# Kernel tuning notes

Measured on AMD Instinct MI355X. Metric: run time of the kernel, lower is better.

The kernel has to match this reference:

```python
import jax, jax.numpy as jnp
import numpy as np
import math

B, W, BINS, H, K = 1, 2048, 1024, 16, 3  # batch, seq (==cropsize), bins, num_bands, kernel


def setup_inputs() -> dict:
    key = jax.random.key(0)
    ks = jax.random.split(key, 7)
    s = 1.0 / math.sqrt(BINS)
    x = jax.random.normal(ks[0], (B, W, BINS), jnp.float32)
    wq = jax.random.normal(ks[1], (BINS, BINS), jnp.float32) * s
    wk = jax.random.normal(ks[2], (BINS, BINS), jnp.float32) * s
    wv = jax.random.normal(ks[3], (BINS, BINS), jnp.float32) * s
    wo = jax.random.normal(ks[4], (BINS, BINS), jnp.float32) * s
    conv_w = jax.random.normal(ks[5], (BINS, 1, K), jnp.float32) * (1.0 / math.sqrt(K))  # depthwise
    er = jax.random.normal(ks[6], (BINS // H, W), jnp.float32)  # relative-position embeddings
    return {"x": x, "wq": wq, "wk": wk, "wv": wv, "wo": wo, "conv_w": conv_w, "er": er}


def _dwconv(x_bwc, w):
    # depthwise Conv1d, 'same' padding (pad=1, k=3). x: [b,w,c], kernel: [c,1,K]
    y = jax.lax.conv_general_dilated(
        x_bwc.transpose(0, 2, 1), w, window_strides=(1,), padding=[(1, 1)],
        feature_group_count=x_bwc.shape[-1], dimension_numbers=("NCH", "OIH", "NCH"))
    return y.transpose(0, 2, 1)


def reference(x, wq, wk, wv, wo, conv_w, er):
    b, w, c = x.shape
    h = H
    d = c // h
    # NOTE: original torch code applies q_conv to q, k AND v (k_conv/v_conv unused).
    q = _dwconv(x @ wq, conv_w).reshape(b, w, h, d).transpose(0, 2, 1, 3)   # [b,h,w,d]
    k = _dwconv(x @ wk, conv_w).reshape(b, w, h, d).transpose(0, 2, 3, 1)   # [b,h,d,w]
    v = _dwconv(x @ wv, conv_w).reshape(b, w, h, d).transpose(0, 2, 1, 3)   # [b,h,w,d]
    # relative-position skewing trick (Music-Transformer style)
    qe = jnp.einsum("bhwd,dr->bhwr", q, er)                                  # [b,h,w,cropsize]
    p = jnp.pad(qe, ((0, 0), (0, 0), (0, 0), (1, 0))).transpose(0, 1, 3, 2)[:, :, 1:, :]  # [b,h,w,w]
    qk = (jnp.einsum("bhwd,bhdk->bhwk", q, k) + p) / math.sqrt(c)
    a = jax.nn.softmax(qk, axis=-1)
    out = jnp.einsum("bhwk,bhkd->bhwd", a, v).transpose(0, 2, 1, 3).reshape(b, w, c)
    return out @ wo
```

## Files before the change

### kernel.cpp

```cpp
#include <hip/hip_runtime.h>
#include <hip/hip_bf16.h>

typedef __attribute__((ext_vector_type(8))) short short8;
typedef __attribute__((ext_vector_type(4))) float floatx4;

__device__ __forceinline__ float bf2f(unsigned short b) {
    union { unsigned int u; float f; } v; v.u = ((unsigned int)b) << 16; return v.f;
}
__device__ __forceinline__ unsigned short f2bf(float f) {
    union { float f; unsigned int u; } v; v.f = f;
    unsigned int r = v.u + 0x7fffu + ((v.u >> 16) & 1u);
    return (unsigned short)(r >> 16);
}
__device__ __forceinline__ unsigned int pk2bf(float a, float b) {
    __hip_bfloat162 h = __float22bfloat162_rn(make_float2(a, b));
    union { __hip_bfloat162 h; unsigned int u; } v; v.h = h; return v.u;
}

union Pack16 { uint4 v[2]; unsigned short u[16]; };
__device__ __forceinline__ void cvt16(const float* __restrict__ src, float s, Pack16& t) {
    float tmp[16];
    *(float4*)&tmp[0]  = ((const float4*)src)[0];
    *(float4*)&tmp[4]  = ((const float4*)src)[1];
    *(float4*)&tmp[8]  = ((const float4*)src)[2];
    *(float4*)&tmp[12] = ((const float4*)src)[3];
#pragma unroll
    for (int i = 0; i < 16; i++) t.u[i] = f2bf(tmp[i] * s);
}

#define MFMA16(a, b, c) __builtin_amdgcn_mfma_f32_16x16x32_bf16((a), (b), (c), 0, 0, 0)

template<bool A_F32, bool BT_PRE, bool C_F32>
__global__ __launch_bounds__(256) void gemm128(
    const void* __restrict__ Ap,
    const void* __restrict__ B0, const void* __restrict__ B1, const void* __restrict__ B2,
    void* __restrict__ C0, void* __restrict__ C1, void* __restrict__ C2,
    int M, int N, int K)
{
    __shared__ __align__(16) unsigned short As[128][72];
    __shared__ __align__(16) unsigned short Bs[128][72];
    const int tid = threadIdx.x;
    const int sel = blockIdx.x >> 3;
    const int n0  = (blockIdx.x & 7) * 128;
    const int m0  = blockIdx.y * 128;
    const void* Bp = (sel == 0) ? B0 : (sel == 1) ? B1 : B2;
    void*       Cp = (sel == 0) ? C0 : (sel == 1) ? C1 : C2;

    const int wv = tid >> 6, lane = tid & 63;
    const int quad = lane >> 4, l15 = lane & 15;
    const int wm0 = (wv >> 1) * 64, wn0 = (wv & 1) * 64;

    floatx4 acc[4][4] = {};

    for (int k0 = 0; k0 < K; k0 += 64) {
        __syncthreads();
        {
            const int r = tid >> 2, c = (tid & 3) * 16;
#pragma unroll
            for (int p = 0; p < 2; p++) {
                const int row = p * 64 + r;
                if (A_F32) {
                    Pack16 t;
                    cvt16((const float*)Ap + (size_t)(m0 + row) * K + k0 + c, 1.0f, t);
                    *(uint4*)&As[row][c]     = t.v[0];
                    *(uint4*)&As[row][c + 8] = t.v[1];
                } else {
                    const uint4* a = (const uint4*)((const unsigned short*)Ap +
                                                    (size_t)(m0 + row) * K + k0 + c);
                    uint4 x0 = a[0], x1 = a[1];
                    *(uint4*)&As[row][c]     = x0;
                    *(uint4*)&As[row][c + 8] = x1;
                }
            }
        }
        if (BT_PRE) {
            const int r = tid >> 2, c = (tid & 3) * 16;
#pragma unroll
            for (int p = 0; p < 2; p++) {
                const int row = p * 64 + r;
                const uint4* b = (const uint4*)((const unsigned short*)Bp +
                                                (size_t)(n0 + row) * K + k0 + c);
                uint4 x0 = b[0], x1 = b[1];
                *(uint4*)&Bs[row][c]     = x0;
                *(uint4*)&Bs[row][c + 8] = x1;
            }
        } else {
            const int kr = tid >> 2, nb = (tid & 3) * 32;
            float t[32];
            const float* b = (const float*)Bp + (size_t)(k0 + kr) * N + n0 + nb;
#pragma unroll
            for (int i = 0; i < 8; i++) *(float4*)&t[i * 4] = ((const float4*)b)[i];
            const int col = ((kr >> 3) ^ ((nb >> 5) & 3)) * 8 + (kr & 7);
#pragma unroll
            for (int j = 0; j < 32; j++) Bs[nb + j][col] = f2bf(t[j]);
        }
        __syncthreads();

#pragma unroll
        for (int ks = 0; ks < 2; ks++) {
            const int kc = ks * 32 + quad * 8;
            short8 af[4], bfr[4];
#pragma unroll
            for (int i = 0; i < 4; i++)
                af[i] = *(const short8*)&As[wm0 + i * 16 + l15][kc];
#pragma unroll
            for (int i = 0; i < 4; i++) {
                int bcol;
                if (BT_PRE) bcol = kc;
                else {
                    const int cx = ((wn0 + i * 16) >> 5) & 3;
                    bcol = ((ks * 4 + quad) ^ cx) * 8;
                }
                bfr[i] = *(const short8*)&Bs[wn0 + i * 16 + l15][bcol];
            }
#pragma unroll
            for (int mt = 0; mt < 4; mt++)
#pragma unroll
                for (int nt = 0; nt < 4; nt++)
                    acc[mt][nt] = MFMA16(af[mt], bfr[nt], acc[mt][nt]);
        }
    }

#pragma unroll
    for (int mt = 0; mt < 4; mt++)
#pragma unroll
        for (int nt = 0; nt < 4; nt++)
#pragma unroll
            for (int r = 0; r < 4; r++) {
                const int row = m0 + wm0 + mt * 16 + quad * 4 + r;
                const int col = n0 + wn0 + nt * 16 + l15;
                if (C_F32)
                    ((float*)Cp)[(size_t)row * N + col] = acc[mt][nt][r];
                else
                    ((unsigned short*)Cp)[(size_t)row * N + col] = f2bf(acc[mt][nt][r]);
            }
}

__global__ __launch_bounds__(256) void wtrans(
    const float* __restrict__ W, unsigned short* __restrict__ WT, int Kd, int Nd)
{
    __shared__ __align__(16) unsigned short T[64][72];
    const int tid = threadIdx.x;
    const int n0 = blockIdx.x * 64, k0 = blockIdx.y * 64;
    {
        const int kr = tid >> 2, nc = (tid & 3) * 16;
        Pack16 t;
        cvt16(W + (size_t)(k0 + kr) * Nd + n0 + nc, 1.0f, t);
#pragma unroll
        for (int j = 0; j < 16; j++) T[nc + j][kr] = t.u[j];
    }
    __syncthreads();
    {
        const int nr = tid >> 2, kc = (tid & 3) * 16;
        uint4 x0 = *(const uint4*)&T[nr][kc];
        uint4 x1 = *(const uint4*)&T[nr][kc + 8];
        uint4* dst = (uint4*)(WT + (size_t)(n0 + nr) * Kd + k0 + kc);
        dst[0] = x0; dst[1] = x1;
    }
}

__global__ __launch_bounds__(256) void conv_qk(
    const unsigned short* __restrict__ in, const float* __restrict__ cw,
    unsigned short* __restrict__ out)
{
    const int idx = blockIdx.x * 256 + threadIdx.x;
    const int w = idx >> 7, c0 = (idx & 127) * 8;
    union { uint4 v; unsigned short u[8]; } a = {}, b, c = {};
    b.v = *(const uint4*)(in + (size_t)w * 1024 + c0);
    if (w > 0)    a.v = *(const uint4*)(in + (size_t)(w - 1) * 1024 + c0);
    if (w < 2047) c.v = *(const uint4*)(in + (size_t)(w + 1) * 1024 + c0);
    union { uint4 v; unsigned short u[8]; } o;
#pragma unroll
    for (int i = 0; i < 8; i++) {
        const float* k3 = cw + (size_t)(c0 + i) * 3;
        o.u[i] = f2bf(bf2f(a.u[i]) * k3[0] + bf2f(b.u[i]) * k3[1] + bf2f(c.u[i]) * k3[2]);
    }
    *(uint4*)(out + (size_t)w * 1024 + c0) = o.v;
}

__global__ __launch_bounds__(256) void conv_vt(
    const unsigned short* __restrict__ in, const float* __restrict__ cw,
    unsigned short* __restrict__ vT)
{
    __shared__ __align__(16) unsigned short T[64][72];
    const int tid = threadIdx.x;
    const int w0 = blockIdx.x * 64, h = blockIdx.y;
    {
        const int wr = tid >> 2, c4 = (tid & 3) * 16;
        const int cg = h * 64 + c4;
        const int w = w0 + wr;
        union { uint4 v[2]; unsigned short u[16]; } a = {}, b, c = {};
        b.v[0] = *(const uint4*)(in + (size_t)w * 1024 + cg);
        b.v[1] = *(const uint4*)(in + (size_t)w * 1024 + cg + 8);
        if (w > 0) {
            a.v[0] = *(const uint4*)(in + (size_t)(w - 1) * 1024 + cg);
            a.v[1] = *(const uint4*)(in + (size_t)(w - 1) * 1024 + cg + 8);
        }
        if (w < 2047) {
            c.v[0] = *(const uint4*)(in + (size_t)(w + 1) * 1024 + cg);
            c.v[1] = *(const uint4*)(in + (size_t)(w + 1) * 1024 + cg + 8);
        }
#pragma unroll
        for (int i = 0; i < 16; i++) {
            const float* k3 = cw + (size_t)(cg + i) * 3;
            T[c4 + i][wr] = f2bf(bf2f(a.u[i]) * k3[0] + bf2f(b.u[i]) * k3[1] +
                                 bf2f(c.u[i]) * k3[2]);
        }
    }
    __syncthreads();
    {
        const int dr = tid >> 2, w4 = (tid & 3) * 16;
        uint4 x0 = *(const uint4*)&T[dr][w4];
        uint4 x1 = *(const uint4*)&T[dr][w4 + 8];
        uint4* dst = (uint4*)(vT + (size_t)(h * 64 + dr) * 2048 + w0 + w4);
        dst[0] = x0; dst[1] = x1;
    }
}

__global__ __launch_bounds__(256, 2) void attn16(
    const unsigned short* __restrict__ qc, const unsigned short* __restrict__ kc,
    const unsigned short* __restrict__ vT, const float* __restrict__ er,
    unsigned short* __restrict__ outp)
{
    __shared__ __align__(16) unsigned char smem[70720];
    unsigned short* Qp = (unsigned short*)smem;

    const int tid = threadIdx.x;
    const int q0 = blockIdx.x * 64, h = blockIdx.y;
    const int wv = tid >> 6, lane = tid & 63;
    const int quad = lane >> 4, l15 = lane & 15;
    const float sc2 = 0.03125f * 1.44269504f;

    {
        const int m = tid >> 2, c4 = (tid & 3) * 16;
        union { uint4 v[2]; unsigned short u[16]; } t;
        t.v[0] = *(const uint4*)(qc + (size_t)(q0 + m) * 1024 + h * 64 + c4);
        t.v[1] = *(const uint4*)(qc + (size_t)(q0 + m) * 1024 + h * 64 + c4 + 8);
#pragma unroll
        for (int i = 0; i < 16; i++) t.u[i] = f2bf(bf2f(t.u[i]) * sc2);
        *(uint4*)&Qp[m * 136 + c4]     = t.v[0];
        *(uint4*)&Qp[m * 136 + c4 + 8] = t.v[1];
        Pack16 e;
        cvt16(er + (size_t)m * 2048 + q0 + c4, sc2, e);
#pragma unroll
        for (int j = 0; j < 16; j++) Qp[(c4 + j) * 136 + 64 + m] = e.u[j];
    }
    __syncthreads();

    short8 Bq[4][4];
#pragma unroll
    for (int qm = 0; qm < 4; qm++)
#pragma unroll
        for (int ks = 0; ks < 4; ks++)
            Bq[qm][ks] = *(const short8*)&Qp[(qm * 16 + l15) * 136 + ks * 32 + quad * 8];

    unsigned short* Ps = (unsigned short*)(smem + 17408 + wv * 9216);

    floatx4 oacc[4][4] = {};
    float lp[4] = {0.f, 0.f, 0.f, 0.f};

    for (int i = 0; i < 8; i++) {
        const int kt = 4 * i + wv;
        floatx4 s[4][4] = {};
#pragma unroll
        for (int half = 0; half < 2; half++) {
            short8 Af[2][4];
#pragma unroll
            for (int kmh = 0; kmh < 2; kmh++)
#pragma unroll
                for (int ks = 0; ks < 4; ks++) {
                    const int row = kt * 64 + (half * 2 + kmh) * 16 + l15;
                    const unsigned short* src = (ks < 2) ? kc : qc;
                    const int col = h * 64 + (ks & 1) * 32 + quad * 8;
                    Af[kmh][ks] = *(const short8*)(src + (size_t)row * 1024 + col);
                }
#pragma unroll
            for (int ks = 0; ks < 4; ks++)
#pragma unroll
                for (int kmh = 0; kmh < 2; kmh++)
#pragma unroll
                    for (int qm = 0; qm < 4; qm++)
                        s[half * 2 + kmh][qm] =
                            MFMA16(Af[kmh][ks], Bq[qm][ks], s[half * 2 + kmh][qm]);
        }

#pragma unroll
        for (int km = 0; km < 4; km++)
#pragma unroll
            for (int qm = 0; qm < 4; qm++) {
                float p0 = exp2f(s[km][qm][0]);
                float p1 = exp2f(s[km][qm][1]);
                float p2 = exp2f(s[km][qm][2]);
                float p3 = exp2f(s[km][qm][3]);
                lp[qm] += (p0 + p1) + (p2 + p3);
                uint2 w;
                w.x = pk2bf(p0, p1);
                w.y = pk2bf(p2, p3);
                *(uint2*)&Ps[(qm * 16 + l15) * 72 + km * 16 + quad * 4] = w;
            }

#pragma unroll
        for (int ks = 0; ks < 2; ks++) {
            short8 Pa[4], Vb[4];
#pragma unroll
            for (int mt = 0; mt < 4; mt++)
                Pa[mt] = *(const short8*)&Ps[(mt * 16 + l15) * 72 + ks * 32 + quad * 8];
#pragma unroll
            for (int nt = 0; nt < 4; nt++)
                Vb[nt] = *(const short8*)(vT + (size_t)(h * 64 + nt * 16 + l15) * 2048 +
                                          kt * 64 + ks * 32 + quad * 8);
#pragma unroll
            for (int mt = 0; mt < 4; mt++)
#pragma unroll
                for (int nt = 0; nt < 4; nt++)
                    oacc[mt][nt] = MFMA16(Pa[mt], Vb[nt], oacc[mt][nt]);
        }
    }

#pragma unroll
    for (int qm = 0; qm < 4; qm++) {
        lp[qm] += __shfl_xor(lp[qm], 16);
        lp[qm] += __shfl_xor(lp[qm], 32);
    }
    __syncthreads();
    float* OfW = (float*)smem + wv * 4420;
#pragma unroll
    for (int mt = 0; mt < 4; mt++)
#pragma unroll
        for (int nt = 0; nt < 4; nt++) {
            floatx4 o = oacc[mt][nt];
            *(float4*)&OfW[(nt * 16 + l15) * 68 + mt * 16 + quad * 4] =
                make_float4(o[0], o[1], o[2], o[3]);
        }
    if (quad == 0) {
#pragma unroll
        for (int qm = 0; qm < 4; qm++) OfW[64 * 68 + qm * 16 + l15] = lp[qm];
    }
    __syncthreads();

    {
        const int d = wv * 16 + l15;
#pragma unroll
        for (int i4 = 0; i4 < 4; i4++) {
            float4 os = make_float4(0.f, 0.f, 0.f, 0.f);
            float4 ls = make_float4(0.f, 0.f, 0.f, 0.f);
#pragma unroll
            for (int s4 = 0; s4 < 4; s4++) {
                const float* R = (const float*)smem + s4 * 4420;
                float4 t  = *(const float4*)&R[d * 68 + quad * 16 + i4 * 4];
                float4 tl = *(const float4*)&R[64 * 68 + quad * 16 + i4 * 4];
                os.x += t.x;  os.y += t.y;  os.z += t.z;  os.w += t.w;
                ls.x += tl.x; ls.y += tl.y; ls.z += tl.z; ls.w += tl.w;
            }
            const int qb4 = quad * 16 + i4 * 4;
            const size_t colb = (size_t)h * 64 + d;
            outp[(size_t)(q0 + qb4 + 0) * 1024 + colb] = f2bf(os.x / ls.x);
            outp[(size_t)(q0 + qb4 + 1) * 1024 + colb] = f2bf(os.y / ls.y);
            outp[(size_t)(q0 + qb4 + 2) * 1024 + colb] = f2bf(os.z / ls.z);
            outp[(size_t)(q0 + qb4 + 3) * 1024 + colb] = f2bf(os.w / ls.w);
        }
    }
}

extern "C" void kernel_launch(void* const* d_in, const int* in_sizes, int n_in,
                              void* d_out, int out_size, void* d_ws, size_t ws_size,
                              hipStream_t stream)
{
    const float* x  = (const float*)d_in[0];
    const float* wq = (const float*)d_in[1];
    const float* wk = (const float*)d_in[2];
    const float* wv = (const float*)d_in[3];
    const float* wo = (const float*)d_in[4];
    const float* cw = (const float*)d_in[5];
    const float* er = (const float*)d_in[6];
    float* out = (float*)d_out;
    unsigned short* ws = (unsigned short*)d_ws;

    const size_t SZ = (size_t)2048 * 1024;
    unsigned short* A0 = ws;
    unsigned short* A1 = ws + SZ;
    unsigned short* A2 = ws + 2 * SZ;
    unsigned short* A3 = ws + 3 * SZ;

    gemm128<true, false, false><<<dim3(24, 16), 256, 0, stream>>>(
        x, wq, wk, wv, A0, A1, A2, 2048, 1024, 1024);
    conv_qk<<<1024, 256, 0, stream>>>(A0, cw, A3);
    conv_qk<<<1024, 256, 0, stream>>>(A1, cw, A0);
    conv_vt<<<dim3(32, 16), 256, 0, stream>>>(A2, cw, A1);
    attn16<<<dim3(32, 16), 256, 0, stream>>>(A3, A0, A1, er, A2);
    wtrans<<<dim3(16, 16), 256, 0, stream>>>(wo, A0, 1024, 1024);
    gemm128<false, true, true><<<dim3(8, 16), 256, 0, stream>>>(
        A2, A0, A0, A0, out, out, out, 2048, 1024, 1024);
}
```

Baseline: 214.5 us.

## Pre-convert x to bf16 and shrink GEMM N-tile to 64 for more blocks

Adds a separate kernel that converts x to bf16 once, instead of each QKV GEMM block re-converting the fp32 A tile for every N-tile. Both GEMMs now use 128x64 tiles, doubling the grid (768 and 256 blocks) so more of the MI355X's compute units get work. The trade-off is an extra launch plus a write and read of x in bf16, and less reuse of each A tile per block.

```diff
diff --git a/kernel.cpp b/kernel.cpp
--- a/kernel.cpp
+++ b/kernel.cpp
@@ -30,27 +30,38 @@
 
 #define MFMA16(a, b, c) __builtin_amdgcn_mfma_f32_16x16x32_bf16((a), (b), (c), 0, 0, 0)
 
-template<bool A_F32, bool BT_PRE, bool C_F32>
-__global__ __launch_bounds__(256) void gemm128(
-    const void* __restrict__ Ap,
+__global__ __launch_bounds__(256) void xcvt(
+    const float* __restrict__ x, unsigned short* __restrict__ xb)
+{
+    const size_t i = ((size_t)blockIdx.x * 256 + threadIdx.x) * 8;
+    float4 a = *(const float4*)(x + i), b = *(const float4*)(x + i + 4);
+    union { uint4 v; unsigned short u[8]; } o;
+    o.u[0] = f2bf(a.x); o.u[1] = f2bf(a.y); o.u[2] = f2bf(a.z); o.u[3] = f2bf(a.w);
+    o.u[4] = f2bf(b.x); o.u[5] = f2bf(b.y); o.u[6] = f2bf(b.z); o.u[7] = f2bf(b.w);
+    *(uint4*)(xb + i) = o.v;
+}
+
+template<bool BT_PRE, bool C_F32>
+__global__ __launch_bounds__(256) void gemmMN(
+    const unsigned short* __restrict__ Abf,
     const void* __restrict__ B0, const void* __restrict__ B1, const void* __restrict__ B2,
     void* __restrict__ C0, void* __restrict__ C1, void* __restrict__ C2,
     int M, int N, int K)
 {
     __shared__ __align__(16) unsigned short As[128][72];
-    __shared__ __align__(16) unsigned short Bs[128][72];
+    __shared__ __align__(16) unsigned short Bs[64][72];
     const int tid = threadIdx.x;
-    const int sel = blockIdx.x >> 3;
-    const int n0  = (blockIdx.x & 7) * 128;
+    const int sel = blockIdx.x >> 4;
+    const int n0  = (blockIdx.x & 15) * 64;
     const int m0  = blockIdx.y * 128;
     const void* Bp = (sel == 0) ? B0 : (sel == 1) ? B1 : B2;
     void*       Cp = (sel == 0) ? C0 : (sel == 1) ? C1 : C2;
 
     const int wv = tid >> 6, lane = tid & 63;
     const int quad = lane >> 4, l15 = lane & 15;
-    const int wm0 = (wv >> 1) * 64, wn0 = (wv & 1) * 64;
-
-    floatx4 acc[4][4] = {};
+    const int wm0 = (wv >> 1) * 64, wn0 = (wv & 1) * 32;
+
+    floatx4 acc[4][2] = {};
 
     for (int k0 = 0; k0 < K; k0 += 64) {
         __syncthreads();
@@ -59,56 +70,45 @@
 #pragma unroll
             for (int p = 0; p < 2; p++) {
                 const int row = p * 64 + r;
-                if (A_F32) {
-                    Pack16 t;
-                    cvt16((const float*)Ap + (size_t)(m0 + row) * K + k0 + c, 1.0f, t);
-                    *(uint4*)&As[row][c]     = t.v[0];
-                    *(uint4*)&As[row][c + 8] = t.v[1];
-                } else {
-                    const uint4* a = (const uint4*)((const unsigned short*)Ap +
-                                                    (size_t)(m0 + row) * K + k0 + c);
-                    uint4 x0 = a[0], x1 = a[1];
-                    *(uint4*)&As[row][c]     = x0;
-                    *(uint4*)&As[row][c + 8] = x1;
-                }
+                const uint4* a = (const uint4*)(Abf + (size_t)(m0 + row) * K + k0 + c);
+                uint4 x0 = a[0], x1 = a[1];
+                *(uint4*)&As[row][c]     = x0;
+                *(uint4*)&As[row][c + 8] = x1;
             }
         }
         if (BT_PRE) {
             const int r = tid >> 2, c = (tid & 3) * 16;
-#pragma unroll
-            for (int p = 0; p < 2; p++) {
-                const int row = p * 64 + r;
-                const uint4* b = (const uint4*)((const unsigned short*)Bp +
-                                                (size_t)(n0 + row) * K + k0 + c);
-                uint4 x0 = b[0], x1 = b[1];
-                *(uint4*)&Bs[row][c]     = x0;
-                *(uint4*)&Bs[row][c + 8] = x1;
-            }
+            const uint4* b = (const uint4*)((const unsigned short*)Bp +
+                                            (size_t)(n0 + r) * K + k0 + c);
+            uint4 x0 = b[0], x1 = b[1];
+            *(uint4*)&Bs[r][c]     = x0;
+            *(uint4*)&Bs[r][c + 8] = x1;
         } else {
-            const int kr = tid >> 2, nb = (tid & 3) * 32;
-            float t[32];
+            const int kr = tid >> 2, nb = (tid & 3) * 16;
+            float t[16];
             const float* b = (const float*)Bp + (size_t)(k0 + kr) * N + n0 + nb;
 #pragma unroll
-            for (int i = 0; i < 8; i++) *(float4*)&t[i * 4] = ((const float4*)b)[i];
-            const int col = ((kr >> 3) ^ ((nb >> 5) & 3)) * 8 + (kr & 7);
-#pragma unroll
-            for (int j = 0; j < 32; j++) Bs[nb + j][col] = f2bf(t[j]);
+            for (int i = 0; i < 4; i++) *(float4*)&t[i * 4] = ((const float4*)b)[i];
+            const int cx = (nb >> 5) & 1;
+            const int colb = ((kr >> 3) ^ cx) * 8 + (kr & 7);
+#pragma unroll
+            for (int j = 0; j < 16; j++) Bs[nb + j][colb] = f2bf(t[j]);
         }
         __syncthreads();
 
 #pragma unroll
         for (int ks = 0; ks < 2; ks++) {
             const int kc = ks * 32 + quad * 8;
-            short8 af[4], bfr[4];
+            short8 af[4], bfr[2];
 #pragma unroll
             for (int i = 0; i < 4; i++)
                 af[i] = *(const short8*)&As[wm0 + i * 16 + l15][kc];
 #pragma unroll
-            for (int i = 0; i < 4; i++) {
+            for (int i = 0; i < 2; i++) {
                 int bcol;
                 if (BT_PRE) bcol = kc;
                 else {
-                    const int cx = ((wn0 + i * 16) >> 5) & 3;
+                    const int cx = ((wn0 + i * 16) >> 5) & 1;
                     bcol = ((ks * 4 + quad) ^ cx) * 8;
                 }
                 bfr[i] = *(const short8*)&Bs[wn0 + i * 16 + l15][bcol];
@@ -116,7 +116,7 @@
 #pragma unroll
             for (int mt = 0; mt < 4; mt++)
 #pragma unroll
-                for (int nt = 0; nt < 4; nt++)
+                for (int nt = 0; nt < 2; nt++)
                     acc[mt][nt] = MFMA16(af[mt], bfr[nt], acc[mt][nt]);
         }
     }
@@ -124,7 +124,7 @@
 #pragma unroll
     for (int mt = 0; mt < 4; mt++)
 #pragma unroll
-        for (int nt = 0; nt < 4; nt++)
+        for (int nt = 0; nt < 2; nt++)
 #pragma unroll
             for (int r = 0; r < 4; r++) {
                 const int row = m0 + wm0 + mt * 16 + quad * 4 + r;
@@ -382,13 +382,14 @@
     unsigned short* A2 = ws + 2 * SZ;
     unsigned short* A3 = ws + 3 * SZ;
 
-    gemm128<true, false, false><<<dim3(24, 16), 256, 0, stream>>>(
-        x, wq, wk, wv, A0, A1, A2, 2048, 1024, 1024);
+    xcvt<<<1024, 256, 0, stream>>>(x, A3);
+    gemmMN<false, false><<<dim3(48, 16), 256, 0, stream>>>(
+        A3, wq, wk, wv, A0, A1, A2, 2048, 1024, 1024);
     conv_qk<<<1024, 256, 0, stream>>>(A0, cw, A3);
     conv_qk<<<1024, 256, 0, stream>>>(A1, cw, A0);
     conv_vt<<<dim3(32, 16), 256, 0, stream>>>(A2, cw, A1);
     attn16<<<dim3(32, 16), 256, 0, stream>>>(A3, A0, A1, er, A2);
     wtrans<<<dim3(16, 16), 256, 0, stream>>>(wo, A0, 1024, 1024);
-    gemm128<false, true, true><<<dim3(8, 16), 256, 0, stream>>>(
+    gemmMN<true, true><<<dim3(16, 16), 256, 0, stream>>>(
         A2, A0, A0, A0, out, out, out, 2048, 1024, 1024);
 }
```

Result: faster. 199.2 us (-7.1%).
